# Kernel tuning notes

Hardware: AMD Instinct MI355X
Metric: run time of the kernel (lower is better)

## Reference

```python
import jax, jax.numpy as jnp
import numpy as np

IMAGE_SIZE = 192
NEAR = 0.1
FAR = 100.0
EPS = 1e-3
BACKGROUND = (0.0, 0.0, 0.0)


def setup_inputs() -> dict:
    key = jax.random.key(0)
    k1, k2, k3, k4 = jax.random.split(key, 4)
    B, F, T = 2, 512, 4
    centers = jax.random.uniform(k1, (B, F, 1, 2), minval=-0.9, maxval=0.9)
    offsets = jax.random.normal(k2, (B, F, 3, 2)) * 0.08
    xy = centers + offsets  # triangle vertices in NDC [-1, 1]
    z = jax.random.uniform(k3, (B, F, 3, 1), minval=1.0, maxval=10.0)  # inside (near, far)
    faces = jnp.concatenate([xy, z], axis=-1).astype(jnp.float32)  # [B,F,3,3]
    textures = jax.random.uniform(k4, (B, F, T, T, T, 3), dtype=jnp.float32)
    return {"faces": faces, "textures": textures}


def _face_inv(v):
    # v: [..., 3 verts, 3 (x,y,z)]. Rows of cofactor matrix / det give barycentric coeffs
    # so that w_k = row_k . (px, py, 1), matching rasterize_cuda's face_inv.
    x0, y0 = v[..., 0, 0], v[..., 0, 1]
    x1, y1 = v[..., 1, 0], v[..., 1, 1]
    x2, y2 = v[..., 2, 0], v[..., 2, 1]
    det = x2 * (y0 - y1) + x0 * (y1 - y2) + x1 * (y2 - y0)
    det = jnp.where(jnp.abs(det) < 1e-12, 1e-12, det)
    rows = jnp.stack([
        y1 - y2, x2 - x1, x1 * y2 - x2 * y1,
        y2 - y0, x0 - x2, x2 * y0 - x0 * y2,
        y0 - y1, x1 - x0, x0 * y1 - x1 * y0], axis=-1)
    return rows.reshape(v.shape[:-2] + (3, 3)) / det[..., None, None]


def _rasterize(faces, textures):
    B, F = faces.shape[:2]
    T = textures.shape[2]
    IS = IMAGE_SIZE
    P = IS * IS
    # pixel centers in NDC, matching (2*i + 1 - is) / is in the CUDA kernel
    coord = (2.0 * jnp.arange(IS, dtype=faces.dtype) + 1.0 - IS) / IS
    yp, xp = jnp.meshgrid(coord, coord, indexing="ij")
    xp = xp.reshape(P)
    yp = yp.reshape(P)
    pc = jnp.stack([xp, yp, jnp.ones((P,), faces.dtype)], axis=-1)  # [P,3]

    x = faces[..., 0]
    y = faces[..., 1]
    z = faces[..., 2]  # [B,F,3]
    # backface culling (skip if (y2-y0)*(x1-x0) < (y1-y0)*(x2-x0))
    front = (y[..., 2] - y[..., 0]) * (x[..., 1] - x[..., 0]) >= \
            (x[..., 2] - x[..., 0]) * (y[..., 1] - y[..., 0])  # [B,F]

    def edge_ok(a, b):
        # pixel on inner side of edge a->b: (yp-ya)*(xb-xa) >= (xp-xa)*(yb-ya)
        return ((yp[None, None, :] - y[..., a:a + 1]) * (x[..., b:b + 1] - x[..., a:a + 1])
                >= (xp[None, None, :] - x[..., a:a + 1]) * (y[..., b:b + 1] - y[..., a:a + 1]))

    inside = edge_ok(0, 1) & edge_ok(1, 2) & edge_ok(2, 0)  # [B,F,P]

    finv = _face_inv(faces)  # [B,F,3,3]
    w = jnp.einsum("bfkc,pc->bfpk", finv, pc)  # barycentric weights [B,F,P,3]
    w = jnp.clip(w, 0.0, 1.0)
    w = w / jnp.maximum(jnp.sum(w, axis=-1, keepdims=True), 1e-12)
    # perspective-correct depth: 1/zp = sum_k w_k / z_k
    zp = 1.0 / jnp.maximum(jnp.einsum("bfpk,bfk->bfp", w, 1.0 / z), 1e-12)
    valid = front[..., None] & inside & (zp > NEAR) & (zp < FAR)
    depth_c = jnp.where(valid, zp, FAR)
    depth_map = jnp.min(depth_c, axis=1)  # z-buffer [B,P]
    fidx = jnp.argmin(depth_c, axis=1)    # winning face per pixel (ties -> lowest index)
    found = depth_map < FAR

    # gather barycentric weights / vertices of the winning face
    wwin = jnp.take_along_axis(w, fidx[:, None, :, None], axis=1)[:, 0]  # [B,P,3]
    vwin = jax.vmap(lambda f, i: f[i])(faces, fidx)  # [B,P,3,3]
    zwin = vwin[..., 2]  # [B,P,3]

    # texture-cube trilinear sampling with perspective-corrected weights
    tif = wwin * (T - 1) * (depth_map[..., None] / zwin)
    tif = jnp.clip(tif, 0.0, T - 1 - EPS)
    tlo_f = jnp.floor(tif)
    frac = tif - tlo_f
    tlo = tlo_f.astype(jnp.int32)
    bits = (jnp.arange(8)[:, None] >> jnp.arange(3)[None, :]) & 1  # [8,3] corner offsets
    idx = tlo[..., None, :] + bits  # [B,P,8,3], in [0, T-1]
    cw = jnp.prod(jnp.where(bits.astype(bool), frac[..., None, :], 1.0 - frac[..., None, :]), axis=-1)  # [B,P,8]
    fsafe = jnp.maximum(fidx, 0)
    flat = ((fsafe[..., None] * T + idx[..., 0]) * T + idx[..., 1]) * T + idx[..., 2]  # [B,P,8]
    texf = textures.reshape(B, F * T * T * T, 3)
    samp = jax.vmap(lambda t, i: t[i])(texf, flat)  # [B,P,8,3]
    rgb = jnp.sum(cw[..., None] * samp, axis=-2)  # [B,P,3]
    bg = jnp.asarray(BACKGROUND, dtype=rgb.dtype)
    rgb = jnp.where(found[..., None], rgb, bg)  # background compositing

    rgb_map = rgb.reshape(B, IS, IS, 3)
    alpha_map = found.astype(faces.dtype).reshape(B, 1, IS, IS)  # single part (part_mask=None)
    depth_out = depth_map.reshape(B, IS, IS)
    return rgb_map, alpha_map, depth_out


def reference(faces, textures):
    return _rasterize(faces, textures)
```

## Files before the change

### kernel.cpp

```cpp
#include <hip/hip_runtime.h>

#define IS     192
#define F_CNT  512
#define TEX    4
#define NEARF  0.1f
#define FARF   100.0f
#define TSZ    8
#define CAP    256

struct alignas(16) FaceData {
    float xmin, xmax, ymin, ymax;
    float x0, y0, x1, y1, x2, y2;
    float f00, f01, f02, f10, f11, f12, f20, f21, f22;
    float iz0, iz1, iz2;
    float z0, z1, z2;
    float pad0, pad1, pad2;
};

__device__ inline FaceData make_face(const float* __restrict__ v) {
    FaceData fd;
    const float x0 = v[0], y0 = v[1], z0 = v[2];
    const float x1 = v[3], y1 = v[4], z1 = v[5];
    const float x2 = v[6], y2 = v[7], z2 = v[8];

    fd.xmin = fminf(x0, fminf(x1, x2));
    fd.xmax = fmaxf(x0, fmaxf(x1, x2));
    fd.ymin = fminf(y0, fminf(y1, y2));
    fd.ymax = fmaxf(y0, fmaxf(y1, y2));
    fd.x0 = x0; fd.y0 = y0; fd.x1 = x1; fd.y1 = y1; fd.x2 = x2; fd.y2 = y2;

    float det = x2 * (y0 - y1) + x0 * (y1 - y2) + x1 * (y2 - y0);
    if (fabsf(det) < 1e-12f) det = 1e-12f;
    fd.f00 = (y1 - y2) / det;
    fd.f01 = (x2 - x1) / det;
    fd.f02 = (x1 * y2 - x2 * y1) / det;
    fd.f10 = (y2 - y0) / det;
    fd.f11 = (x0 - x2) / det;
    fd.f12 = (x2 * y0 - x0 * y2) / det;
    fd.f20 = (y0 - y1) / det;
    fd.f21 = (x1 - x0) / det;
    fd.f22 = (x0 * y1 - x1 * y0) / det;

    fd.iz0 = 1.0f / z0; fd.iz1 = 1.0f / z1; fd.iz2 = 1.0f / z2;
    fd.z0 = z0; fd.z1 = z1; fd.z2 = z2;
    return fd;
}

__global__ __launch_bounds__(64) void raster_kernel(
    const float* __restrict__ faces,
    const float* __restrict__ textures,
    float* __restrict__ out)
{
    __shared__ FaceData sf[CAP];
    __shared__ unsigned short sidx[F_CNT];
    __shared__ int scount;

    const int b   = blockIdx.z;
    const int tx0 = blockIdx.x * TSZ;
    const int ty0 = blockIdx.y * TSZ;
    const int tid = threadIdx.y * TSZ + threadIdx.x;

    if (tid == 0) scount = 0;
    __syncthreads();

    const float xlo = (2.0f * tx0             + 1.0f - IS) / (float)IS;
    const float xhi = (2.0f * (tx0 + TSZ - 1) + 1.0f - IS) / (float)IS;
    const float ylo = (2.0f * ty0             + 1.0f - IS) / (float)IS;
    const float yhi = (2.0f * (ty0 + TSZ - 1) + 1.0f - IS) / (float)IS;

    for (int f = tid; f < F_CNT; f += 64) {
        const float* v = faces + ((size_t)b * F_CNT + f) * 9;
        const float x0 = v[0], y0 = v[1];
        const float x1 = v[3], y1 = v[4];
        const float x2 = v[6], y2 = v[7];

        const bool front = (y2 - y0) * (x1 - x0) >= (x2 - x0) * (y1 - y0);

        const float bxmin = fminf(x0, fminf(x1, x2));
        const float bxmax = fmaxf(x0, fmaxf(x1, x2));
        const float bymin = fminf(y0, fminf(y1, y2));
        const float bymax = fmaxf(y0, fmaxf(y1, y2));

        const bool keep = front &&
                          bxmin <= xhi && bxmax >= xlo &&
                          bymin <= yhi && bymax >= ylo;
        if (keep) {
            const int slot = atomicAdd(&scount, 1);
            sidx[slot] = (unsigned short)f;
            if (slot < CAP) sf[slot] = make_face(v);
        }
    }
    __syncthreads();

    const int px = tx0 + threadIdx.x;
    const int py = ty0 + threadIdx.y;
    const float xp = (2.0f * px + 1.0f - IS) / (float)IS;
    const float yp = (2.0f * py + 1.0f - IS) / (float)IS;

    float best = FARF;
    int bestf = -1;
    float bw0 = 0.0f, bw1 = 0.0f, bw2 = 0.0f;
    float bz0 = 1.0f, bz1 = 1.0f, bz2 = 1.0f;

    auto process = [&](const FaceData& fd, const int f) {
        if (xp < fd.xmin || xp > fd.xmax || yp < fd.ymin || yp > fd.ymax) return;

        const bool in01 = (yp - fd.y0) * (fd.x1 - fd.x0) >= (xp - fd.x0) * (fd.y1 - fd.y0);
        const bool in12 = (yp - fd.y1) * (fd.x2 - fd.x1) >= (xp - fd.x1) * (fd.y2 - fd.y1);
        const bool in20 = (yp - fd.y2) * (fd.x0 - fd.x2) >= (xp - fd.x2) * (fd.y0 - fd.y2);
        if (!(in01 && in12 && in20)) return;

        float w0 = fd.f00 * xp + fd.f01 * yp + fd.f02;
        float w1 = fd.f10 * xp + fd.f11 * yp + fd.f12;
        float w2 = fd.f20 * xp + fd.f21 * yp + fd.f22;
        w0 = fminf(fmaxf(w0, 0.0f), 1.0f);
        w1 = fminf(fmaxf(w1, 0.0f), 1.0f);
        w2 = fminf(fmaxf(w2, 0.0f), 1.0f);
        const float ws = fmaxf(w0 + w1 + w2, 1e-12f);
        w0 = w0 / ws; w1 = w1 / ws; w2 = w2 / ws;

        const float s = w0 * fd.iz0 + w1 * fd.iz1 + w2 * fd.iz2;
        const float zp = 1.0f / fmaxf(s, 1e-12f);

        if (zp > NEARF && zp < FARF) {
            if (zp < best || (zp == best && f < bestf)) {
                best = zp; bestf = f;
                bw0 = w0; bw1 = w1; bw2 = w2;
                bz0 = fd.z0; bz1 = fd.z1; bz2 = fd.z2;
            }
        }
    };

    const int cnt = scount;
    const int ncached = (cnt < CAP) ? cnt : CAP;
    for (int i = 0; i < ncached; ++i)
        process(sf[i], sidx[i]);
    for (int i = CAP; i < cnt; ++i) {
        const int f = sidx[i];
        const FaceData fd = make_face(faces + ((size_t)b * F_CNT + f) * 9);
        process(fd, f);
    }

    float r = 0.0f, g = 0.0f, bc = 0.0f;
    if (bestf >= 0) {
        float t0 = bw0 * 3.0f * (best / bz0);
        float t1 = bw1 * 3.0f * (best / bz1);
        float t2 = bw2 * 3.0f * (best / bz2);
        const float tmax = 2.999f;
        t0 = fminf(fmaxf(t0, 0.0f), tmax);
        t1 = fminf(fmaxf(t1, 0.0f), tmax);
        t2 = fminf(fmaxf(t2, 0.0f), tmax);
        const float fl0 = floorf(t0), fl1 = floorf(t1), fl2 = floorf(t2);
        const float fr0 = t0 - fl0, fr1 = t1 - fl1, fr2 = t2 - fl2;
        const int i0 = (int)fl0, i1 = (int)fl1, i2 = (int)fl2;

        const float* tex = textures + ((size_t)b * F_CNT + bestf) * (TEX * TEX * TEX * 3);
        #pragma unroll
        for (int c = 0; c < 8; ++c) {
            const int b0 = c & 1, b1 = (c >> 1) & 1, b2 = (c >> 2) & 1;
            const float cw = (b0 ? fr0 : 1.0f - fr0)
                           * (b1 ? fr1 : 1.0f - fr1)
                           * (b2 ? fr2 : 1.0f - fr2);
            const float* sp = tex + (((size_t)(i0 + b0) * TEX + (i1 + b1)) * TEX + (i2 + b2)) * 3;
            r  += cw * sp[0];
            g  += cw * sp[1];
            bc += cw * sp[2];
        }
    }

    const size_t pix = (size_t)py * IS + px;
    const size_t bp  = (size_t)b * IS * IS + pix;

    out[bp * 3 + 0] = r;
    out[bp * 3 + 1] = g;
    out[bp * 3 + 2] = bc;

    float* alpha = out + (size_t)2 * IS * IS * 3;
    alpha[bp] = (bestf >= 0) ? 1.0f : 0.0f;

    float* depth = alpha + (size_t)2 * IS * IS;
    depth[bp] = best;
}

extern "C" void kernel_launch(void* const* d_in, const int* in_sizes, int n_in,
                              void* d_out, int out_size, void* d_ws, size_t ws_size,
                              hipStream_t stream) {
    const float* faces    = (const float*)d_in[0];
    const float* textures = (const float*)d_in[1];
    float* out = (float*)d_out;

    const int B = in_sizes[0] / (F_CNT * 9);

    dim3 grid(IS / TSZ, IS / TSZ, B);
    dim3 block(TSZ, TSZ, 1);
    raster_kernel<<<grid, block, 0, stream>>>(faces, textures, out);
}
```

Baseline: 16.28 us.

## Use 32x16-pixel blocks of 512 threads with one face per thread in binning

Tiles grow from 8x8 pixels with 64 threads to 32x16 pixels with 512 threads, so each thread bins exactly one face and the loop over faces disappears. The grid shrinks from 576 blocks to 72 blocks in total, which cuts redundant face loading and binning across blocks. The trade-offs are fewer blocks to spread over the GPU's many CUs and more candidate faces per tile. More faces per tile can overflow the 256-entry shared cache and push work onto the slow uncached path, and the wider tile puts more faces that a given pixel never touches into each thread's candidate loop.

Result: faster. 14.31 us (-12.1%).

```diff
diff --git a/kernel.cpp b/kernel.cpp
--- a/kernel.cpp
+++ b/kernel.cpp
@@ -5,7 +5,8 @@
 #define TEX    4
 #define NEARF  0.1f
 #define FARF   100.0f
-#define TSZ    8
+#define RW     32
+#define RH     16
 #define CAP    256
 
 struct alignas(16) FaceData {
@@ -46,7 +47,7 @@
     return fd;
 }
 
-__global__ __launch_bounds__(64) void raster_kernel(
+__global__ __launch_bounds__(RW * RH) void raster_kernel(
     const float* __restrict__ faces,
     const float* __restrict__ textures,
     float* __restrict__ out)
@@ -56,19 +57,20 @@
     __shared__ int scount;
 
     const int b   = blockIdx.z;
-    const int tx0 = blockIdx.x * TSZ;
-    const int ty0 = blockIdx.y * TSZ;
-    const int tid = threadIdx.y * TSZ + threadIdx.x;
+    const int rx0 = blockIdx.x * RW;
+    const int ry0 = blockIdx.y * RH;
+    const int tid = threadIdx.y * RW + threadIdx.x;
 
     if (tid == 0) scount = 0;
     __syncthreads();
 
-    const float xlo = (2.0f * tx0             + 1.0f - IS) / (float)IS;
-    const float xhi = (2.0f * (tx0 + TSZ - 1) + 1.0f - IS) / (float)IS;
-    const float ylo = (2.0f * ty0             + 1.0f - IS) / (float)IS;
-    const float yhi = (2.0f * (ty0 + TSZ - 1) + 1.0f - IS) / (float)IS;
+    const float xlo = (2.0f * rx0            + 1.0f - IS) / (float)IS;
+    const float xhi = (2.0f * (rx0 + RW - 1) + 1.0f - IS) / (float)IS;
+    const float ylo = (2.0f * ry0            + 1.0f - IS) / (float)IS;
+    const float yhi = (2.0f * (ry0 + RH - 1) + 1.0f - IS) / (float)IS;
 
-    for (int f = tid; f < F_CNT; f += 64) {
+    {
+        const int f = tid;
         const float* v = faces + ((size_t)b * F_CNT + f) * 9;
         const float x0 = v[0], y0 = v[1];
         const float x1 = v[3], y1 = v[4];
@@ -92,8 +94,8 @@
     }
     __syncthreads();
 
-    const int px = tx0 + threadIdx.x;
-    const int py = ty0 + threadIdx.y;
+    const int px = rx0 + threadIdx.x;
+    const int py = ry0 + threadIdx.y;
     const float xp = (2.0f * px + 1.0f - IS) / (float)IS;
     const float yp = (2.0f * py + 1.0f - IS) / (float)IS;
 
@@ -191,7 +193,7 @@
 
     const int B = in_sizes[0] / (F_CNT * 9);
 
-    dim3 grid(IS / TSZ, IS / TSZ, B);
-    dim3 block(TSZ, TSZ, 1);
+    dim3 grid(IS / RW, IS / RH, B);
+    dim3 block(RW, RH, 1);
     raster_kernel<<<grid, block, 0, stream>>>(faces, textures, out);
 }
```
